# Performance work log

Hardware: AMD Instinct MI355X
Metric: run time of the kernel (lower is better)

## Reference

```python
import jax, jax.numpy as jnp
import numpy as np

RADIUS = 2.0
DECAY = 1.0


def setup_inputs() -> dict:
    key = jax.random.key(0)
    k1, k2 = jax.random.split(key)
    x = jax.random.normal(k1, (2048, 16), dtype=jnp.float32)
    data = jax.random.normal(k2, (65536, 16), dtype=jnp.float32)
    return {"x": x, "data": data}


def reference(x, data):
    # Brute-force L2 nearest-neighbor (faiss IndexFlatL2 / IVF nlist=1 == exact search)
    # dist2[q, n] = ||x_q - data_n||^2, via the expansion trick.
    x2 = jnp.sum(x * x, axis=1, keepdims=True)            # [Nq, 1]
    d2 = jnp.sum(data * data, axis=1)                      # [Nd]
    dist2 = x2 + d2[None, :] - 2.0 * (x @ data.T)          # [Nq, Nd] -- dominant traffic
    nn2 = jnp.maximum(jnp.min(dist2, axis=1), 0.0)         # clamp tiny negatives from cancellation
    dist = jnp.sqrt(jnp.maximum(nn2, 1e-12))               # sqrt of squared L2, squeeze(k=1)

    # bump_above(dist, RADIUS, DECAY):
    #   inside mask: exp(decay / (d^2 - r^2)) / exp(-decay / r^2)
    #   outside: 0
    r2 = RADIUS * RADIUS
    mask = jnp.abs(dist) < RADIUS
    denom = jnp.where(mask, dist * dist - r2, -1.0)        # safe denom outside mask
    bump = jnp.where(mask, jnp.exp(DECAY / denom + DECAY / r2), 0.0)
    return bump
```

## Files before the change

### kernel.cpp

```cpp
#include <hip/hip_runtime.h>
#include <float.h>
#include <math.h>

constexpr int NQ = 2048;
constexpr int ND = 65536;
constexpr int D  = 16;

constexpr int SCH   = 64;
constexpr int CP    = ND / SCH;
constexpr int TPW   = CP / 32;
constexpr int NPAIR = TPW / 2;

typedef short bf16x8 __attribute__((ext_vector_type(8)));
typedef float f32x16 __attribute__((ext_vector_type(16)));

__device__ __forceinline__ unsigned short f2bf(float f) {
    unsigned u = __float_as_uint(f);
    u += 0x7FFFu + ((u >> 16) & 1u);
    return (unsigned short)(u >> 16);
}
__device__ __forceinline__ float bf2f(unsigned short h) {
    return __uint_as_float(((unsigned)h) << 16);
}

__global__ __launch_bounds__(256) void pack_data(const float* __restrict__ data,
                                                 unsigned short* __restrict__ Ppk,
                                                 float* __restrict__ nhf) {
    const int lb  = blockIdx.x;
    const int xcd = lb & 7;
    const int r   = lb >> 3;
    const int q4  = r & 3;
    const int cg  = r >> 2;
    const int cy  = xcd + 8 * cg;
    const int p   = cy * CP + q4 * 256 + threadIdx.x;

    const float4* r4 = (const float4*)(data + (size_t)p * D);
    float4 a = r4[0], b = r4[1], c = r4[2], e = r4[3];
    float v[16] = {a.x, a.y, a.z, a.w, b.x, b.y, b.z, b.w,
                   c.x, c.y, c.z, c.w, e.x, e.y, e.z, e.w};
    unsigned short hi[16], lo[16];
    float n = 0.f;
#pragma unroll
    for (int k = 0; k < 16; ++k) {
        n = fmaf(v[k], v[k], n);
        unsigned short h = f2bf(v[k]);
        hi[k] = h;
        lo[k] = f2bf(v[k] - bf2f(h));
    }
    const int t  = p >> 5;
    const int cc = p & 31;
    unsigned short* tb = Ppk + (size_t)t * 1024;
    const uint4* h4 = (const uint4*)hi;
    const uint4* l4 = (const uint4*)lo;
    *(uint4*)(tb +        cc * 8) = h4[0];
    *(uint4*)(tb + 256 +  cc * 8) = h4[1];
    *(uint4*)(tb + 512 +  cc * 8) = l4[0];
    *(uint4*)(tb + 768 +  cc * 8) = l4[1];
    nhf[p] = -0.5f * n;
}

__global__ __launch_bounds__(256, 2) void knn_mfma(const float* __restrict__ x,
                                                   const unsigned short* __restrict__ Ppk,
                                                   const float* __restrict__ nhf,
                                                   float* __restrict__ part) {
    const int lb  = blockIdx.x;
    const int xcd = lb & 7;
    const int rr  = lb >> 3;
    const int qx  = rr & 7;
    const int cg  = rr >> 3;
    const int cy  = xcd + 8 * cg;

    const int tid  = threadIdx.x;
    const int w    = tid >> 6;
    const int l    = tid & 63;
    const int half = l >> 5;
    const int n31  = l & 31;
    const int qbase = qx * 256 + w * 64;
    const int pbase = cy * CP;

    bf16x8 axh0, axl0, axh1, axl1;
    {
        const float* xr0 = x + (size_t)(qbase + n31) * D + half * 8;
        float4 a0 = *(const float4*)xr0;
        float4 a1 = *(const float4*)(xr0 + 4);
        const float xv0[8] = {a0.x, a0.y, a0.z, a0.w, a1.x, a1.y, a1.z, a1.w};
#pragma unroll
        for (int k = 0; k < 8; ++k) {
            unsigned short h = f2bf(xv0[k]);
            axh0[k] = (short)h;
            axl0[k] = (short)f2bf(xv0[k] - bf2f(h));
        }
        const float* xr1 = x + (size_t)(qbase + 32 + n31) * D + half * 8;
        float4 b0 = *(const float4*)xr1;
        float4 b1 = *(const float4*)(xr1 + 4);
        const float xv1[8] = {b0.x, b0.y, b0.z, b0.w, b1.x, b1.y, b1.z, b1.w};
#pragma unroll
        for (int k = 0; k < 8; ++k) {
            unsigned short h = f2bf(xv1[k]);
            axh1[k] = (short)h;
            axl1[k] = (short)f2bf(xv1[k] - bf2f(h));
        }
    }

    const unsigned short* bp = Ppk + (size_t)(pbase >> 5) * 1024 + l * 8;
    const float*          np = nhf + pbase + n31;

#define LDH(t) (*(const bf16x8*)(bp + (size_t)(t) * 1024))
#define LDL(t) (*(const bf16x8*)(bp + (size_t)(t) * 1024 + 512))
#define LDN(t) (np[(size_t)(t) * 32])

    f32x16 rbest0, rbest1;
#pragma unroll
    for (int r = 0; r < 16; ++r) { rbest0[r] = -FLT_MAX; rbest1[r] = -FLT_MAX; }

    auto compute_pair = [&](bf16x8 h0, bf16x8 l0, float n0,
                            bf16x8 h1, bf16x8 l1, float n1) {
        f32x16 c00, c01, c10, c11;
#pragma unroll
        for (int r = 0; r < 16; ++r) {
            c00[r] = n0; c01[r] = n1; c10[r] = n0; c11[r] = n1;
        }
        c00 = __builtin_amdgcn_mfma_f32_32x32x16_bf16(axh0, h0, c00, 0, 0, 0);
        c01 = __builtin_amdgcn_mfma_f32_32x32x16_bf16(axh0, h1, c01, 0, 0, 0);
        c10 = __builtin_amdgcn_mfma_f32_32x32x16_bf16(axh1, h0, c10, 0, 0, 0);
        c11 = __builtin_amdgcn_mfma_f32_32x32x16_bf16(axh1, h1, c11, 0, 0, 0);
        c00 = __builtin_amdgcn_mfma_f32_32x32x16_bf16(axl0, h0, c00, 0, 0, 0);
        c01 = __builtin_amdgcn_mfma_f32_32x32x16_bf16(axl0, h1, c01, 0, 0, 0);
        c10 = __builtin_amdgcn_mfma_f32_32x32x16_bf16(axl1, h0, c10, 0, 0, 0);
        c11 = __builtin_amdgcn_mfma_f32_32x32x16_bf16(axl1, h1, c11, 0, 0, 0);
        c00 = __builtin_amdgcn_mfma_f32_32x32x16_bf16(axh0, l0, c00, 0, 0, 0);
        c01 = __builtin_amdgcn_mfma_f32_32x32x16_bf16(axh0, l1, c01, 0, 0, 0);
        c10 = __builtin_amdgcn_mfma_f32_32x32x16_bf16(axh1, l0, c10, 0, 0, 0);
        c11 = __builtin_amdgcn_mfma_f32_32x32x16_bf16(axh1, l1, c11, 0, 0, 0);
#pragma unroll
        for (int r = 0; r < 16; ++r) {
            rbest0[r] = fmaxf(rbest0[r], fmaxf(c00[r], c01[r]));
            rbest1[r] = fmaxf(rbest1[r], fmaxf(c10[r], c11[r]));
        }
    };

    bf16x8 Ah0 = LDH(0), Al0 = LDL(0), Ah1 = LDH(1), Al1 = LDL(1);
    float  An0 = LDN(0), An1 = LDN(1);
    bf16x8 Bh0, Bl0, Bh1, Bl1;
    float  Bn0, Bn1;

    for (int p = 0; p < NPAIR; p += 2) {
        const int tB = (p + 1) * 2;
        Bh0 = LDH(tB);     Bl0 = LDL(tB);     Bn0 = LDN(tB);
        Bh1 = LDH(tB + 1); Bl1 = LDL(tB + 1); Bn1 = LDN(tB + 1);
        compute_pair(Ah0, Al0, An0, Ah1, Al1, An1);
        if (p + 2 < NPAIR) {
            const int tA = (p + 2) * 2;
            Ah0 = LDH(tA);     Al0 = LDL(tA);     An0 = LDN(tA);
            Ah1 = LDH(tA + 1); Al1 = LDL(tA + 1); An1 = LDN(tA + 1);
        }
        compute_pair(Bh0, Bl0, Bn0, Bh1, Bl1, Bn1);
    }
#undef LDH
#undef LDL
#undef LDN

#pragma unroll
    for (int r = 0; r < 16; ++r) {
        float v0 = rbest0[r];
        v0 = fmaxf(v0, __shfl_xor(v0, 1, 32));
        v0 = fmaxf(v0, __shfl_xor(v0, 2, 32));
        v0 = fmaxf(v0, __shfl_xor(v0, 4, 32));
        v0 = fmaxf(v0, __shfl_xor(v0, 8, 32));
        v0 = fmaxf(v0, __shfl_xor(v0, 16, 32));
        rbest0[r] = v0;
        float v1 = rbest1[r];
        v1 = fmaxf(v1, __shfl_xor(v1, 1, 32));
        v1 = fmaxf(v1, __shfl_xor(v1, 2, 32));
        v1 = fmaxf(v1, __shfl_xor(v1, 4, 32));
        v1 = fmaxf(v1, __shfl_xor(v1, 8, 32));
        v1 = fmaxf(v1, __shfl_xor(v1, 16, 32));
        rbest1[r] = v1;
    }
    if (n31 == 0) {
        float* pp = part + (size_t)cy * NQ + qbase + 4 * half;
#pragma unroll
        for (int r = 0; r < 16; ++r) pp[(r & 3) + 8 * (r >> 2)] = rbest0[r];
        pp += 32;
#pragma unroll
        for (int r = 0; r < 16; ++r) pp[(r & 3) + 8 * (r >> 2)] = rbest1[r];
    }
}

__global__ __launch_bounds__(256) void knn_final(const float* __restrict__ x,
                                                 const float* __restrict__ part,
                                                 float* __restrict__ out) {
    const int q = blockIdx.x * 256 + threadIdx.x;
    const float4* xr = (const float4*)(x + (size_t)q * D);
    float4 a = xr[0], b = xr[1], c = xr[2], e = xr[3];
    float x2 = a.x * a.x;
    x2 = fmaf(a.y, a.y, x2); x2 = fmaf(a.z, a.z, x2); x2 = fmaf(a.w, a.w, x2);
    x2 = fmaf(b.x, b.x, x2); x2 = fmaf(b.y, b.y, x2); x2 = fmaf(b.z, b.z, x2); x2 = fmaf(b.w, b.w, x2);
    x2 = fmaf(c.x, c.x, x2); x2 = fmaf(c.y, c.y, x2); x2 = fmaf(c.z, c.z, x2); x2 = fmaf(c.w, c.w, x2);
    x2 = fmaf(e.x, e.x, x2); x2 = fmaf(e.y, e.y, x2); x2 = fmaf(e.z, e.z, x2); x2 = fmaf(e.w, e.w, x2);

    float mbest = -FLT_MAX;
#pragma unroll
    for (int cI = 0; cI < SCH; ++cI) mbest = fmaxf(mbest, part[(size_t)cI * NQ + q]);

    float nn2  = fmaxf(fmaf(-2.f, mbest, x2), 0.f);
    float dist = sqrtf(fmaxf(nn2, 1e-12f));
    float bump = 0.f;
    if (dist < 2.0f) {
        float denom = dist * dist - 4.0f;
        bump = expf(1.0f / denom + 0.25f);
    }
    out[q] = bump;
}

__global__ __launch_bounds__(256) void neg_half_norms(const float* __restrict__ data,
                                                      float* __restrict__ nhn) {
    const int p = blockIdx.x * 256 + threadIdx.x;
    const float4* r = (const float4*)(data + (size_t)p * D);
    float4 a = r[0], b = r[1], c = r[2], e = r[3];
    float n = a.x * a.x;
    n = fmaf(a.y, a.y, n); n = fmaf(a.z, a.z, n); n = fmaf(a.w, a.w, n);
    n = fmaf(b.x, b.x, n); n = fmaf(b.y, b.y, n); n = fmaf(b.z, b.z, n); n = fmaf(b.w, b.w, n);
    n = fmaf(c.x, c.x, n); n = fmaf(c.y, c.y, n); n = fmaf(c.z, c.z, n); n = fmaf(c.w, c.w, n);
    n = fmaf(e.x, e.x, n); n = fmaf(e.y, e.y, n); n = fmaf(e.z, e.z, n); n = fmaf(e.w, e.w, n);
    nhn[p] = -0.5f * n;
}

__global__ __launch_bounds__(256) void knn_partial_fb(const float* __restrict__ x,
                                                      const float* __restrict__ data,
                                                      const float* __restrict__ nhn,
                                                      float* __restrict__ part, int cp) {
    const int q     = blockIdx.x * 256 + threadIdx.x;
    const int pbase = blockIdx.y * cp;
    const float4* xr = (const float4*)(x + (size_t)q * D);
    const float4 xa = xr[0], xb = xr[1], xc = xr[2], xd = xr[3];
    const float* dp = data + (size_t)pbase * D;
    const float* np = nhn + pbase;
    float best = -FLT_MAX;
    for (int i = 0; i < cp; i += 4) {
#pragma unroll
        for (int j = 0; j < 4; ++j) {
            const float* r  = dp + (size_t)(i + j) * D;
            const float  hn = np[i + j];
            float ca = xa.x * r[0];
            ca = fmaf(xa.y, r[1], ca);  ca = fmaf(xa.z, r[2], ca);  ca = fmaf(xa.w, r[3], ca);
            ca = fmaf(xb.x, r[4], ca);  ca = fmaf(xb.y, r[5], ca);  ca = fmaf(xb.z, r[6], ca);
            ca = fmaf(xb.w, r[7], ca);
            float cb = fmaf(xc.x, r[8], hn);
            cb = fmaf(xc.y, r[9],  cb); cb = fmaf(xc.z, r[10], cb); cb = fmaf(xc.w, r[11], cb);
            cb = fmaf(xd.x, r[12], cb); cb = fmaf(xd.y, r[13], cb); cb = fmaf(xd.z, r[14], cb);
            cb = fmaf(xd.w, r[15], cb);
            best = fmaxf(best, ca + cb);
        }
    }
    part[(size_t)blockIdx.y * NQ + q] = best;
}

__global__ __launch_bounds__(256) void knn_final_fb(const float* __restrict__ x,
                                                    const float* __restrict__ part,
                                                    float* __restrict__ out, int S) {
    const int q = blockIdx.x * 256 + threadIdx.x;
    const float4* xr = (const float4*)(x + (size_t)q * D);
    float4 a = xr[0], b = xr[1], c = xr[2], e = xr[3];
    float x2 = a.x * a.x;
    x2 = fmaf(a.y, a.y, x2); x2 = fmaf(a.z, a.z, x2); x2 = fmaf(a.w, a.w, x2);
    x2 = fmaf(b.x, b.x, x2); x2 = fmaf(b.y, b.y, x2); x2 = fmaf(b.z, b.z, x2); x2 = fmaf(b.w, b.w, x2);
    x2 = fmaf(c.x, c.x, x2); x2 = fmaf(c.y, c.y, x2); x2 = fmaf(c.z, c.z, x2); x2 = fmaf(c.w, c.w, x2);
    x2 = fmaf(e.x, e.x, x2); x2 = fmaf(e.y, e.y, x2); x2 = fmaf(e.z, e.z, x2); x2 = fmaf(e.w, e.w, x2);
    float mb = -FLT_MAX;
    for (int cI = 0; cI < S; ++cI) mb = fmaxf(mb, part[(size_t)cI * NQ + q]);
    float nn2  = fmaxf(fmaf(-2.f, mb, x2), 0.f);
    float dist = sqrtf(fmaxf(nn2, 1e-12f));
    float bump = 0.f;
    if (dist < 2.0f) {
        float denom = dist * dist - 4.0f;
        bump = expf(1.0f / denom + 0.25f);
    }
    out[q] = bump;
}

extern "C" void kernel_launch(void* const* d_in, const int* in_sizes, int n_in,
                              void* d_out, int out_size, void* d_ws, size_t ws_size,
                              hipStream_t stream) {
    const float* x    = (const float*)d_in[0];
    const float* data = (const float*)d_in[1];
    float* out = (float*)d_out;

    const size_t off_nhf  = (size_t)ND * 32 * 2;
    const size_t off_part = off_nhf + (size_t)ND * 4;
    const size_t needed   = off_part + (size_t)SCH * NQ * 4;

    if (ws_size >= needed) {
        unsigned short* Ppk = (unsigned short*)d_ws;
        float* nhf  = (float*)((char*)d_ws + off_nhf);
        float* part = (float*)((char*)d_ws + off_part);

        pack_data<<<ND / 256, 256, 0, stream>>>(data, Ppk, nhf);
        knn_mfma<<<8 * SCH, 256, 0, stream>>>(x, Ppk, nhf, part);
        knn_final<<<NQ / 256, 256, 0, stream>>>(x, part, out);
    } else {
        int S = 32;
        while (S > 1 && (size_t)(ND + S * NQ) * sizeof(float) > ws_size) S >>= 1;
        const int cp = ND / S;
        float* nhn  = (float*)d_ws;
        float* part = (float*)d_ws + ND;
        neg_half_norms<<<ND / 256, 256, 0, stream>>>(data, nhn);
        knn_partial_fb<<<dim3(NQ / 256, S), 256, 0, stream>>>(x, data, nhn, part, cp);
        knn_final_fb<<<NQ / 256, 256, 0, stream>>>(x, part, out, S);
    }
}
```

Measured before the change: 79.99 us.

## Stage packed data chunk in LDS and share across the block's four waves

Each block now loads its full 64KB packed data chunk (bf16 hi/lo split) into shared memory once with coalesced 16-byte copies, then syncs. The four waves read B fragments from LDS instead of each streaming the same chunk from global memory. The norm terms are preloaded into a 32-entry register array. This cuts duplicate global/L2 traffic across waves, but it drops the software-pipelined register prefetch, uses 64KB of LDS per block, which may limit occupancy, and adds a block-wide barrier before compute.

```diff
diff --git a/kernel.cpp b/kernel.cpp
--- a/kernel.cpp
+++ b/kernel.cpp
@@ -9,7 +9,6 @@
 constexpr int SCH   = 64;
 constexpr int CP    = ND / SCH;
 constexpr int TPW   = CP / 32;
-constexpr int NPAIR = TPW / 2;
 
 typedef short bf16x8 __attribute__((ext_vector_type(8)));
 typedef float f32x16 __attribute__((ext_vector_type(16)));
@@ -78,6 +77,22 @@
     const int qbase = qx * 256 + w * 64;
     const int pbase = cy * CP;
 
+    __shared__ __align__(16) unsigned short sP[32768];
+
+    const char* gC = (const char*)Ppk + (size_t)cy * 65536;
+    char*       lC = (char*)sP;
+#pragma unroll
+    for (int i = 0; i < 16; ++i) {
+        const int off = i * 4096 + tid * 16;
+        uint4 v = *(const uint4*)(gC + off);
+        *(uint4*)(lC + off) = v;
+    }
+
+    const float* np = nhf + pbase + n31;
+    float nv[32];
+#pragma unroll
+    for (int t = 0; t < 32; ++t) nv[t] = np[t * 32];
+
     bf16x8 axh0, axl0, axh1, axl1;
     {
         const float* xr0 = x + (size_t)(qbase + n31) * D + half * 8;
@@ -102,12 +117,11 @@
         }
     }
 
-    const unsigned short* bp = Ppk + (size_t)(pbase >> 5) * 1024 + l * 8;
-    const float*          np = nhf + pbase + n31;
-
-#define LDH(t) (*(const bf16x8*)(bp + (size_t)(t) * 1024))
-#define LDL(t) (*(const bf16x8*)(bp + (size_t)(t) * 1024 + 512))
-#define LDN(t) (np[(size_t)(t) * 32])
+    __syncthreads();
+
+    const unsigned short* lp = sP + l * 8;
+#define LDH(t) (*(const bf16x8*)(lp + (size_t)(t) * 1024))
+#define LDL(t) (*(const bf16x8*)(lp + (size_t)(t) * 1024 + 512))
 
     f32x16 rbest0, rbest1;
 #pragma unroll
@@ -139,26 +153,12 @@
         }
     };
 
-    bf16x8 Ah0 = LDH(0), Al0 = LDL(0), Ah1 = LDH(1), Al1 = LDL(1);
-    float  An0 = LDN(0), An1 = LDN(1);
-    bf16x8 Bh0, Bl0, Bh1, Bl1;
-    float  Bn0, Bn1;
-
-    for (int p = 0; p < NPAIR; p += 2) {
-        const int tB = (p + 1) * 2;
-        Bh0 = LDH(tB);     Bl0 = LDL(tB);     Bn0 = LDN(tB);
-        Bh1 = LDH(tB + 1); Bl1 = LDL(tB + 1); Bn1 = LDN(tB + 1);
-        compute_pair(Ah0, Al0, An0, Ah1, Al1, An1);
-        if (p + 2 < NPAIR) {
-            const int tA = (p + 2) * 2;
-            Ah0 = LDH(tA);     Al0 = LDL(tA);     An0 = LDN(tA);
-            Ah1 = LDH(tA + 1); Al1 = LDL(tA + 1); An1 = LDN(tA + 1);
-        }
-        compute_pair(Bh0, Bl0, Bn0, Bh1, Bl1, Bn1);
+    for (int p = 0; p < TPW; p += 2) {
+        compute_pair(LDH(p),     LDL(p),     nv[p],
+                     LDH(p + 1), LDL(p + 1), nv[p + 1]);
     }
 #undef LDH
 #undef LDL
-#undef LDN
 
 #pragma unroll
     for (int r = 0; r < 16; ++r) {
```

Result: faster. 75.98 us (-5.0%).
